# Optimization experiments

Measured on AMD Instinct MI355X. Metric: run time of the kernel, lower is better.

Reference implementation:

```python
import jax, jax.numpy as jnp
import numpy as np

EPS = 1e-9
NEG_BIG = -1e9


def setup_inputs() -> dict:
    key = jax.random.key(0)
    kq, kk, kv, km = jax.random.split(key, 4)
    B, S, D = 2, 2048, 1024
    q = jax.random.normal(kq, (B, S, D), dtype=jnp.float32)
    k = jax.random.normal(kk, (B, S, D), dtype=jnp.float32)
    v = jax.random.normal(kv, (B, S, D), dtype=jnp.float32)
    mask = jax.random.randint(km, (S, S), 0, 2, dtype=jnp.int32)
    return {"q": q, "k": k, "v": v, "mask": mask, "num_heads": 16}


def _split_heads(x, num_heads):
    B, S, D = x.shape
    # [B, S, D] -> [B, H, S, dh]
    return x.reshape(B, S, num_heads, D // num_heads).transpose(0, 2, 1, 3)


def reference(q, k, v, mask, num_heads):
    B, S, D = q.shape
    dh = D // num_heads
    scale = dh ** (-0.5)
    qh = _split_heads(q, num_heads)  # [B,H,S,dh]
    kh = _split_heads(k, num_heads)
    vh = _split_heads(v, num_heads)
    # pairwise euclidean distance (cdist, p=2): sqrt(|q|^2 + |k|^2 - 2 q.k)
    q2 = jnp.sum(qh * qh, axis=-1)  # [B,H,S]
    k2 = jnp.sum(kh * kh, axis=-1)  # [B,H,S]
    qk = jnp.einsum("bhqd,bhkd->bhqk", qh, kh)
    d2 = q2[..., :, None] + k2[..., None, :] - 2.0 * qk
    dist = jnp.sqrt(jnp.maximum(d2, 0.0)) * scale  # [B,H,S,S]
    attn = 1.0 / (dist + EPS)
    attn = attn + mask.astype(jnp.float32)[None, None] * NEG_BIG
    attn = jax.nn.softmax(attn, axis=-1)
    # dropout is identity in eval / p=0.0
    x = jnp.einsum("bhqk,bhkd->bhqd", attn, vh)
    # [B,H,S,dh] -> [B,S,D]
    return x.transpose(0, 2, 1, 3).reshape(B, S, D)
```

## Files before the change

kernel.cpp:

```cpp
#include <hip/hip_runtime.h>
#include <hip/hip_bf16.h>
#include <math.h>

namespace {

constexpr int S  = 2048;
constexpr int D  = 1024;
constexpr int H  = 16;
constexpr int DH = 64;
constexpr int QB = 32;
constexpr int KT = 64;
constexpr float NEG_BIG = -1e9f;

typedef __attribute__((ext_vector_type(8))) short short8;
typedef __attribute__((ext_vector_type(4))) float f32x4;

union Frag {
  unsigned u[4];
  short8 v;
};

constexpr size_t ELEMS   = (size_t)2 * H * S * DH;
constexpr size_t OFF_KHI  = 0;
constexpr size_t OFF_KLO  = ELEMS * 2;
constexpr size_t OFF_VTHI = ELEMS * 4;
constexpr size_t OFF_VTLO = ELEMS * 6;
constexpr size_t OFF_K2   = ELEMS * 8;
constexpr size_t WS_NEED  = ELEMS * 8 + (size_t)2 * H * S * 4;

__device__ __forceinline__ unsigned fbits(float f) { return __float_as_uint(f); }
__device__ __forceinline__ unsigned packhi(unsigned a, unsigned b) {
  return (a >> 16) | (b & 0xFFFF0000u);
}
__device__ __forceinline__ void split2(float e, float o, unsigned& hi, unsigned& lo) {
  const unsigned ue = fbits(e), uo = fbits(o);
  hi = packhi(ue, uo);
  const float he = __uint_as_float(ue & 0xFFFF0000u);
  const float ho = __uint_as_float(uo & 0xFFFF0000u);
  lo = packhi(fbits(e - he), fbits(o - ho));
}

__device__ __forceinline__ unsigned bf16bits(float f) {
  __hip_bfloat16 h = __float2bfloat16(f);
  unsigned short us;
  __builtin_memcpy(&us, &h, 2);
  return (unsigned)us;
}
__device__ __forceinline__ unsigned pk2(float e, float o) {
  return bf16bits(e) | (bf16bits(o) << 16);
}

#define MFMA16 __builtin_amdgcn_mfma_f32_16x16x32_bf16


__global__ __launch_bounds__(256) void prep_k(const float* __restrict__ kin,
                                              short8* __restrict__ khi,
                                              short8* __restrict__ klo,
                                              float* __restrict__ k2) {
  const int t = blockIdx.x * 256 + (int)threadIdx.x;
  const int c = t & 7, h = (t >> 3) & 15, s = (t >> 7) & 2047, b = t >> 18;
  const float* p = kin + ((size_t)(b * S + s)) * D + h * DH + c * 8;
  float f[8];
  *(float4*)f       = *(const float4*)p;
  *(float4*)(f + 4) = *(const float4*)(p + 4);
  Frag hi, lo;
  float ss = 0.f;
#pragma unroll
  for (int w2 = 0; w2 < 4; ++w2) {
    split2(f[2 * w2], f[2 * w2 + 1], hi.u[w2], lo.u[w2]);
    ss += f[2 * w2] * f[2 * w2] + f[2 * w2 + 1] * f[2 * w2 + 1];
  }
  const size_t o8 = ((size_t)((b * 16 + h) * S + s)) * 8 + c;
  khi[o8] = hi.v;
  klo[o8] = lo.v;
  ss += __shfl_xor(ss, 1, 8);
  ss += __shfl_xor(ss, 2, 8);
  ss += __shfl_xor(ss, 4, 8);
  if (c == 0) k2[(b * 16 + h) * S + s] = ss;
}

__global__ __launch_bounds__(256) void prep_vt(const float* __restrict__ vin,
                                               short8* __restrict__ vthi,
                                               short8* __restrict__ vtlo) {
  __shared__ float Vs[64][65];
  const int blk = blockIdx.x;
  const int st = blk & 31, h = (blk >> 5) & 15, b = blk >> 9;
  const int t = (int)threadIdx.x;
  {
    const int r = t >> 2, cq = t & 3;
    const float* p = vin + ((size_t)(b * S + st * 64 + r)) * D + h * DH + cq * 16;
#pragma unroll
    for (int i = 0; i < 4; ++i)
      *(float4*)&Vs[r][cq * 16 + i * 4] = *(const float4*)(p + i * 4);
  }
  __syncthreads();
  const int d = t >> 2, sq = t & 3;
  Frag h0, h1, l0, l1;
#pragma unroll
  for (int j = 0; j < 4; ++j)
    split2(Vs[sq * 16 + 2 * j][d], Vs[sq * 16 + 2 * j + 1][d], h0.u[j], l0.u[j]);
#pragma unroll
  for (int j = 0; j < 4; ++j)
    split2(Vs[sq * 16 + 8 + 2 * j][d], Vs[sq * 16 + 8 + 2 * j + 1][d], h1.u[j], l1.u[j]);
  const size_t o8 = (((size_t)(b * 16 + h) * DH + d) * S + st * 64 + sq * 16) / 8;
  vthi[o8]     = h0.v;
  vthi[o8 + 1] = h1.v;
  vtlo[o8]     = l0.v;
  vtlo[o8 + 1] = l1.v;
}


__global__ __launch_bounds__(256, 2)
void euclid_attn_fast(const float* __restrict__ qg,
                      const int* __restrict__ maskg,
                      const short8* __restrict__ khi,
                      const short8* __restrict__ klo,
                      const short8* __restrict__ vthi,
                      const short8* __restrict__ vtlo,
                      const float* __restrict__ k2g,
                      float* __restrict__ outg) {
  const int bx = blockIdx.x;
  const int bh = blockIdx.y;
  const int b  = bh >> 4;
  const int tid  = (int)threadIdx.x;
  const int w    = tid >> 6;
  const int lane = tid & 63;
  const int x    = lane & 15;
  const int g    = lane >> 4;
  const int q0   = bx * QB;

  const float* Qb = qg + ((size_t)b * S + q0) * D + (bh & 15) * DH;

  const int idxk0 = (20 * g) * 4;
  const int idxe0 = (32 * (g & 1) + x) * 4;

  Frag Qhi[2][2], Qlo[2][2];
  float q2v[2];
#pragma unroll
  for (int nf = 0; nf < 2; ++nf) {
    float ss = 0.f;
#pragma unroll
    for (int s = 0; s < 2; ++s) {
      const float* p = Qb + (16 * nf + x) * D + 32 * s + 8 * g;
      float f[8];
      *(float4*)(f)     = *(const float4*)(p);
      *(float4*)(f + 4) = *(const float4*)(p + 4);
#pragma unroll
      for (int w2 = 0; w2 < 4; ++w2) {
        split2(f[2 * w2], f[2 * w2 + 1], Qhi[nf][s].u[w2], Qlo[nf][s].u[w2]);
        ss += f[2 * w2] * f[2 * w2] + f[2 * w2 + 1] * f[2 * w2 + 1];
      }
    }
    ss += __shfl_xor(ss, 16);
    ss += __shfl_xor(ss, 32);
    q2v[nf] = ss;
  }

  f32x4 acc[2][4] = {};
  float m_[2] = {-1e30f, -1e30f};
  float l_[2] = {0.f, 0.f};

  const int mrow0 = (q0 + x) * S;

  for (int t = 0; t < (S / KT) / 4; ++t) {
    const int k0 = (w + 4 * t) * KT;

    f32x4 dv[4][2];
    float rmax[2] = {-3e38f, -3e38f};

#pragma unroll
    for (int mf = 0; mf < 4; ++mf) {
      float mar[2][4];
#pragma unroll
      for (int nf = 0; nf < 2; ++nf) {
        const int4 mi =
            *(const int4*)(maskg + (size_t)mrow0 + 16 * nf * S + k0 + 16 * mf + 4 * g);
        mar[nf][0] = (float)mi.x; mar[nf][1] = (float)mi.y;
        mar[nf][2] = (float)mi.z; mar[nf][3] = (float)mi.w;
      }

      const size_t kb8 = ((size_t)bh * S + k0 + 16 * mf + x) * 8;
      Frag kh[2], kl[2];
      kh[0].v = khi[kb8 + g];
      kh[1].v = khi[kb8 + 4 + g];
      kl[0].v = klo[kb8 + g];
      kl[1].v = klo[kb8 + 4 + g];

      const float4 k2r = *(const float4*)(k2g + (size_t)bh * S + k0 + 16 * mf + 4 * g);
      const float k2a[4] = {k2r.x, k2r.y, k2r.z, k2r.w};

#pragma unroll
      for (int nf = 0; nf < 2; ++nf) {
        f32x4 d = {0.f, 0.f, 0.f, 0.f};
        d = MFMA16(kl[0].v, Qhi[nf][0].v, d, 0, 0, 0);
        d = MFMA16(kh[0].v, Qlo[nf][0].v, d, 0, 0, 0);
        d = MFMA16(kh[0].v, Qhi[nf][0].v, d, 0, 0, 0);
        d = MFMA16(kl[1].v, Qhi[nf][1].v, d, 0, 0, 0);
        d = MFMA16(kh[1].v, Qlo[nf][1].v, d, 0, 0, 0);
        d = MFMA16(kh[1].v, Qhi[nf][1].v, d, 0, 0, 0);
        dv[mf][nf] = d;
      }

#pragma unroll
      for (int nf = 0; nf < 2; ++nf)
#pragma unroll
        for (int r = 0; r < 4; ++r) {
          float d2 = q2v[nf] + k2a[r] - 2.f * dv[mf][nf][r];
          d2 = fmaxf(d2, 1e-8f);
          float a = 8.f * rsqrtf(d2);
          a = fmaf(mar[nf][r], NEG_BIG, a);
          dv[mf][nf][r] = a;
          rmax[nf] = fmaxf(rmax[nf], a);
        }
    }

    float corr_s[2];
#pragma unroll
    for (int nf = 0; nf < 2; ++nf) {
      float rm = rmax[nf];
      rm = fmaxf(rm, __shfl_xor(rm, 16));
      rm = fmaxf(rm, __shfl_xor(rm, 32));
      float mn   = fmaxf(m_[nf], rm);
      float corr = __expf(m_[nf] - mn);
      m_[nf] = mn;
      float rs = 0.f;
#pragma unroll
      for (int mf = 0; mf < 4; ++mf)
#pragma unroll
        for (int r = 0; r < 4; ++r) {
          float pp = __expf(dv[mf][nf][r] - mn);
          dv[mf][nf][r] = pp;
          rs += pp;
        }
      rs += __shfl_xor(rs, 16);
      rs += __shfl_xor(rs, 32);
      l_[nf] = l_[nf] * corr + rs;
      corr_s[nf] = corr;
    }

#pragma unroll
    for (int mo = 0; mo < 2; ++mo)
#pragma unroll
      for (int r = 0; r < 4; ++r) {
        float cT = __int_as_float(__builtin_amdgcn_ds_bpermute(
            idxk0 + 4 * r, __float_as_int(corr_s[mo])));
#pragma unroll
        for (int nv = 0; nv < 4; ++nv)
          acc[mo][nv][r] *= cT;
      }

    unsigned P2h[2][4][2], P2l[2][4][2];
#pragma unroll
    for (int nf = 0; nf < 2; ++nf)
#pragma unroll
      for (int mf = 0; mf < 4; ++mf)
#pragma unroll
        for (int c = 0; c < 2; ++c)
          split2(dv[mf][nf][2 * c], dv[mf][nf][2 * c + 1],
                 P2h[nf][mf][c], P2l[nf][mf][c]);

    Frag afh[2][2], afl[2][2];
    const bool upper = (g >= 2);
#pragma unroll
    for (int nf = 0; nf < 2; ++nf)
#pragma unroll
      for (int s2 = 0; s2 < 2; ++s2)
#pragma unroll
        for (int w4 = 0; w4 < 4; ++w4) {
          const int c = w4 & 1;
          const int idx = idxe0 + 64 * (w4 >> 1);
          int a0 = __builtin_amdgcn_ds_bpermute(idx, (int)P2h[nf][2 * s2][c]);
          int a1 = __builtin_amdgcn_ds_bpermute(idx, (int)P2h[nf][2 * s2 + 1][c]);
          afh[nf][s2].u[w4] = (unsigned)(upper ? a1 : a0);
          int b0 = __builtin_amdgcn_ds_bpermute(idx, (int)P2l[nf][2 * s2][c]);
          int b1 = __builtin_amdgcn_ds_bpermute(idx, (int)P2l[nf][2 * s2 + 1][c]);
          afl[nf][s2].u[w4] = (unsigned)(upper ? b1 : b0);
        }

#pragma unroll
    for (int nv = 0; nv < 4; ++nv)
#pragma unroll
      for (int s2 = 0; s2 < 2; ++s2) {
        const size_t vt8 =
            (((size_t)bh * DH + 16 * nv + x) * S + k0 + 32 * s2 + 8 * g) / 8;
        Frag vh, vl;
        vh.v = vthi[vt8];
        vl.v = vtlo[vt8];
#pragma unroll
        for (int mo = 0; mo < 2; ++mo) {
          f32x4 a = acc[mo][nv];
          a = MFMA16(afl[mo][s2].v, vh.v, a, 0, 0, 0);
          a = MFMA16(afh[mo][s2].v, vl.v, a, 0, 0, 0);
          a = MFMA16(afh[mo][s2].v, vh.v, a, 0, 0, 0);
          acc[mo][nv] = a;
        }
      }
  }

  __shared__ float accs[4][QB][DH];
  __shared__ float mls[4][2][QB];
#pragma unroll
  for (int mo = 0; mo < 2; ++mo)
#pragma unroll
    for (int nv = 0; nv < 4; ++nv)
#pragma unroll
      for (int r = 0; r < 4; ++r)
        accs[w][16 * mo + 4 * g + r][16 * nv + x] = acc[mo][nv][r];
  if (g == 0) {
#pragma unroll
    for (int nf = 0; nf < 2; ++nf) {
      mls[w][0][16 * nf + x] = m_[nf];
      mls[w][1][16 * nf + x] = l_[nf];
    }
  }
  __syncthreads();

  const int qq  = tid >> 3;
  const int dh0 = (tid & 7) * 8;
  float M = -3e38f;
#pragma unroll
  for (int ww = 0; ww < 4; ++ww) M = fmaxf(M, mls[ww][0][qq]);
  float L = 0.f;
  float sw[4];
#pragma unroll
  for (int ww = 0; ww < 4; ++ww) {
    sw[ww] = __expf(mls[ww][0][qq] - M);
    L += sw[ww] * mls[ww][1][qq];
  }
  const float inv = 1.f / L;
  float o[8] = {};
#pragma unroll
  for (int ww = 0; ww < 4; ++ww)
#pragma unroll
    for (int jj = 0; jj < 8; ++jj)
      o[jj] += sw[ww] * accs[ww][qq][dh0 + jj];
#pragma unroll
  for (int jj = 0; jj < 8; ++jj) o[jj] *= inv;
  float* op = outg + ((size_t)b * S + q0 + qq) * D + (bh & 15) * DH + dh0;
  *(float4*)(op)     = *(float4*)(o);
  *(float4*)(op + 4) = *(float4*)(o + 4);
}


__global__ __launch_bounds__(256, 2)
void euclid_attn_mfma(const float* __restrict__ qg,
                      const float* __restrict__ kg,
                      const float* __restrict__ vg,
                      const int*   __restrict__ maskg,
                      float*       __restrict__ outg) {
  const int bx = blockIdx.x;
  const int bh = blockIdx.y;
  const int b  = bh >> 4, h = bh & 15;
  const int tid  = (int)threadIdx.x;
  const int w    = tid >> 6;
  const int lane = tid & 63;
  const int x    = lane & 15;
  const int g    = lane >> 4;
  const int q0   = bx * QB;

  const float* Qb = qg + ((size_t)b * S + q0) * D + h * DH;
  const float* Kb = kg + (size_t)b * S * D + h * DH;
  const float* Vb = vg + (size_t)b * S * D + h * DH;

  const int idxk0 = (20 * g) * 4;
  const int idxe0 = (32 * (g & 1) + x) * 4;

  Frag Qhi[2][2], Qlo[2][2];
  float q2v[2];
#pragma unroll
  for (int nf = 0; nf < 2; ++nf) {
    float ss = 0.f;
#pragma unroll
    for (int s = 0; s < 2; ++s) {
      const float* p = Qb + (16 * nf + x) * D + 32 * s + 8 * g;
      float f[8];
      *(float4*)(f)     = *(const float4*)(p);
      *(float4*)(f + 4) = *(const float4*)(p + 4);
#pragma unroll
      for (int w2 = 0; w2 < 4; ++w2) {
        float e = f[2*w2], o = f[2*w2+1];
        unsigned hw = pk2(e, o);
        Qhi[nf][s].u[w2] = hw;
        float he = __uint_as_float(hw << 16);
        float ho = __uint_as_float(hw & 0xFFFF0000u);
        Qlo[nf][s].u[w2] = pk2(e - he, o - ho);
        ss += e * e + o * o;
      }
    }
    ss += __shfl_xor(ss, 16);
    ss += __shfl_xor(ss, 32);
    q2v[nf] = ss;
  }

  f32x4 acc[2][4] = {};
  float m_[2] = {-1e30f, -1e30f};
  float l_[2] = {0.f, 0.f};

  const int mrow0 = (q0 + x) * S;

  for (int t = 0; t < (S / KT) / 4; ++t) {
    const int k0 = (w + 4 * t) * KT;

    f32x4 dv[4][2];
    float rmax[2] = {-3e38f, -3e38f};

#pragma unroll
    for (int mf = 0; mf < 4; ++mf) {
      float msk[2][4];
#pragma unroll
      for (int nf = 0; nf < 2; ++nf)
#pragma unroll
        for (int r = 0; r < 4; ++r)
          msk[nf][r] =
              (float)maskg[mrow0 + 16 * nf * S + k0 + 16 * mf + 4 * g + r];

      const float* kp = Kb + (k0 + 16 * mf + x) * D + 8 * g;
      float f[16];
      *(float4*)(f)      = *(const float4*)(kp);
      *(float4*)(f + 4)  = *(const float4*)(kp + 4);
      *(float4*)(f + 8)  = *(const float4*)(kp + 32);
      *(float4*)(f + 12) = *(const float4*)(kp + 36);
      Frag khi[2], klo[2];
      float ss = 0.f;
#pragma unroll
      for (int s = 0; s < 2; ++s)
#pragma unroll
        for (int w2 = 0; w2 < 4; ++w2) {
          float e = f[8*s + 2*w2], o = f[8*s + 2*w2 + 1];
          unsigned hw = pk2(e, o);
          khi[s].u[w2] = hw;
          float he = __uint_as_float(hw << 16);
          float ho = __uint_as_float(hw & 0xFFFF0000u);
          klo[s].u[w2] = pk2(e - he, o - ho);
          ss += e * e + o * o;
        }
      ss += __shfl_xor(ss, 16);
      ss += __shfl_xor(ss, 32);
      float k2r[4];
#pragma unroll
      for (int r = 0; r < 4; ++r)
        k2r[r] = __int_as_float(
            __builtin_amdgcn_ds_bpermute(idxk0 + 4 * r, __float_as_int(ss)));

#pragma unroll
      for (int nf = 0; nf < 2; ++nf) {
        f32x4 d = {0.f, 0.f, 0.f, 0.f};
        d = MFMA16(klo[0].v, Qhi[nf][0].v, d, 0, 0, 0);
        d = MFMA16(khi[0].v, Qlo[nf][0].v, d, 0, 0, 0);
        d = MFMA16(khi[0].v, Qhi[nf][0].v, d, 0, 0, 0);
        d = MFMA16(klo[1].v, Qhi[nf][1].v, d, 0, 0, 0);
        d = MFMA16(khi[1].v, Qlo[nf][1].v, d, 0, 0, 0);
        d = MFMA16(khi[1].v, Qhi[nf][1].v, d, 0, 0, 0);
        dv[mf][nf] = d;
      }

#pragma unroll
      for (int nf = 0; nf < 2; ++nf)
#pragma unroll
        for (int r = 0; r < 4; ++r) {
          float d2 = q2v[nf] + k2r[r] - 2.f * dv[mf][nf][r];
          d2 = fmaxf(d2, 1e-8f);
          float a = 8.f * rsqrtf(d2);
          a = fmaf(msk[nf][r], NEG_BIG, a);
          dv[mf][nf][r] = a;
          rmax[nf] = fmaxf(rmax[nf], a);
        }
    }

    float corr_s[2];
#pragma unroll
    for (int nf = 0; nf < 2; ++nf) {
      float rm = rmax[nf];
      rm = fmaxf(rm, __shfl_xor(rm, 16));
      rm = fmaxf(rm, __shfl_xor(rm, 32));
      float mn   = fmaxf(m_[nf], rm);
      float corr = __expf(m_[nf] - mn);
      m_[nf] = mn;
      float rs = 0.f;
#pragma unroll
      for (int mf = 0; mf < 4; ++mf)
#pragma unroll
        for (int r = 0; r < 4; ++r) {
          float pp = __expf(dv[mf][nf][r] - mn);
          dv[mf][nf][r] = pp;
          rs += pp;
        }
      rs += __shfl_xor(rs, 16);
      rs += __shfl_xor(rs, 32);
      l_[nf] = l_[nf] * corr + rs;
      corr_s[nf] = corr;
    }

#pragma unroll
    for (int mo = 0; mo < 2; ++mo)
#pragma unroll
      for (int r = 0; r < 4; ++r) {
        float cT = __int_as_float(__builtin_amdgcn_ds_bpermute(
            idxk0 + 4 * r, __float_as_int(corr_s[mo])));
#pragma unroll
        for (int nv = 0; nv < 4; ++nv)
          acc[mo][nv][r] *= cT;
      }

    unsigned P2h[2][4][2], P2l[2][4][2];
#pragma unroll
    for (int nf = 0; nf < 2; ++nf)
#pragma unroll
      for (int mf = 0; mf < 4; ++mf)
#pragma unroll
        for (int c = 0; c < 2; ++c) {
          float p0 = dv[mf][nf][2*c], p1 = dv[mf][nf][2*c+1];
          unsigned hw = pk2(p0, p1);
          P2h[nf][mf][c] = hw;
          float he = __uint_as_float(hw << 16);
          float ho = __uint_as_float(hw & 0xFFFF0000u);
          P2l[nf][mf][c] = pk2(p0 - he, p1 - ho);
        }

    Frag afh[2][2], afl[2][2];
    const bool upper = (g >= 2);
#pragma unroll
    for (int nf = 0; nf < 2; ++nf)
#pragma unroll
      for (int s2 = 0; s2 < 2; ++s2)
#pragma unroll
        for (int w4 = 0; w4 < 4; ++w4) {
          const int c = w4 & 1;
          const int idx = idxe0 + 64 * (w4 >> 1);
          int a0 = __builtin_amdgcn_ds_bpermute(idx, (int)P2h[nf][2*s2][c]);
          int a1 = __builtin_amdgcn_ds_bpermute(idx, (int)P2h[nf][2*s2+1][c]);
          afh[nf][s2].u[w4] = (unsigned)(upper ? a1 : a0);
          int b0 = __builtin_amdgcn_ds_bpermute(idx, (int)P2l[nf][2*s2][c]);
          int b1 = __builtin_amdgcn_ds_bpermute(idx, (int)P2l[nf][2*s2+1][c]);
          afl[nf][s2].u[w4] = (unsigned)(upper ? b1 : b0);
        }

#pragma unroll
    for (int nv = 0; nv < 4; ++nv)
#pragma unroll
      for (int s2 = 0; s2 < 2; ++s2) {
        const float* vp = Vb + (k0 + 32 * s2 + 8 * g) * D + 16 * nv + x;
        float f[8];
#pragma unroll
        for (int j = 0; j < 8; ++j) f[j] = vp[j * D];
        Frag vh, vl;
#pragma unroll
        for (int w2 = 0; w2 < 4; ++w2) {
          float e = f[2*w2], o = f[2*w2+1];
          unsigned hw = pk2(e, o);
          vh.u[w2] = hw;
          float he = __uint_as_float(hw << 16);
          float ho = __uint_as_float(hw & 0xFFFF0000u);
          vl.u[w2] = pk2(e - he, o - ho);
        }
#pragma unroll
        for (int mo = 0; mo < 2; ++mo) {
          f32x4 a = acc[mo][nv];
          a = MFMA16(afl[mo][s2].v, vh.v, a, 0, 0, 0);
          a = MFMA16(afh[mo][s2].v, vl.v, a, 0, 0, 0);
          a = MFMA16(afh[mo][s2].v, vh.v, a, 0, 0, 0);
          acc[mo][nv] = a;
        }
      }
  }

  __shared__ float accs[4][QB][DH];
  __shared__ float mls[4][2][QB];
#pragma unroll
  for (int mo = 0; mo < 2; ++mo)
#pragma unroll
    for (int nv = 0; nv < 4; ++nv)
#pragma unroll
      for (int r = 0; r < 4; ++r)
        accs[w][16 * mo + 4 * g + r][16 * nv + x] = acc[mo][nv][r];
  if (g == 0) {
#pragma unroll
    for (int nf = 0; nf < 2; ++nf) {
      mls[w][0][16 * nf + x] = m_[nf];
      mls[w][1][16 * nf + x] = l_[nf];
    }
  }
  __syncthreads();

  const int qq  = tid >> 3;
  const int dh0 = (tid & 7) * 8;
  float M = -3e38f;
#pragma unroll
  for (int ww = 0; ww < 4; ++ww) M = fmaxf(M, mls[ww][0][qq]);
  float L = 0.f;
  float sw[4];
#pragma unroll
  for (int ww = 0; ww < 4; ++ww) {
    sw[ww] = __expf(mls[ww][0][qq] - M);
    L += sw[ww] * mls[ww][1][qq];
  }
  const float inv = 1.f / L;
  float o[8] = {};
#pragma unroll
  for (int ww = 0; ww < 4; ++ww)
#pragma unroll
    for (int jj = 0; jj < 8; ++jj)
      o[jj] += sw[ww] * accs[ww][qq][dh0 + jj];
#pragma unroll
  for (int jj = 0; jj < 8; ++jj) o[jj] *= inv;
  float* op = outg + ((size_t)b * S + q0 + qq) * D + h * DH + dh0;
  *(float4*)(op)     = *(float4*)(o);
  *(float4*)(op + 4) = *(float4*)(o + 4);
}

}

extern "C" void kernel_launch(void* const* d_in, const int* in_sizes, int n_in,
                              void* d_out, int out_size, void* d_ws, size_t ws_size,
                              hipStream_t stream) {
  const float* q    = (const float*)d_in[0];
  const float* k    = (const float*)d_in[1];
  const float* v    = (const float*)d_in[2];
  const int*   mask = (const int*)d_in[3];
  float* out = (float*)d_out;

  const int B = in_sizes[0] / (S * D);
  dim3 grid(S / QB, B * H);
  dim3 block(256);

  if (B == 2 && d_ws != nullptr && ws_size >= WS_NEED) {
    char* ws = (char*)d_ws;
    short8* khi  = (short8*)(ws + OFF_KHI);
    short8* klo  = (short8*)(ws + OFF_KLO);
    short8* vthi = (short8*)(ws + OFF_VTHI);
    short8* vtlo = (short8*)(ws + OFF_VTLO);
    float*  k2   = (float*)(ws + OFF_K2);
    prep_k<<<2048, 256, 0, stream>>>(k, khi, klo, k2);
    prep_vt<<<1024, 256, 0, stream>>>(v, vthi, vtlo);
    euclid_attn_fast<<<grid, block, 0, stream>>>(q, mask, khi, klo, vthi, vtlo,
                                                 k2, out);
  } else {
    euclid_attn_mfma<<<grid, block, 0, stream>>>(q, k, v, mask, out);
  }
}
```

Measured before the change: 413.5 us.

## Use permlane swaps for reductions, lazy softmax rescale, raise occupancy

Replaces shfl_xor reductions and ds_bpermute fragment transposes with permlane32/permlane16 swap builtins when available, so these cross-lane moves avoid LDS-based permutes. Adds a lazy online-softmax rescale that skips updating the running max and rescaling the accumulators unless some row's new max exceeds the old one by more than 8. Raises the launch-bounds occupancy hint from 2 to 4 blocks per SIMD, which limits registers per thread and may cause spills. The lazy threshold keeps the exponent bounded but lets values exceed 1 before normalization.

```diff
diff --git a/kernel.cpp b/kernel.cpp
--- a/kernel.cpp
+++ b/kernel.cpp
@@ -8,7 +8,6 @@
 constexpr int D  = 1024;
 constexpr int H  = 16;
 constexpr int DH = 64;
-constexpr int QB = 32;
 constexpr int KT = 64;
 constexpr float NEG_BIG = -1e9f;
 
@@ -28,6 +27,13 @@
 constexpr size_t OFF_K2   = ELEMS * 8;
 constexpr size_t WS_NEED  = ELEMS * 8 + (size_t)2 * H * S * 4;
 
+#if __has_builtin(__builtin_amdgcn_permlane32_swap) && \
+    __has_builtin(__builtin_amdgcn_permlane16_swap)
+#define HAVE_PLSWAP 1
+#else
+#define HAVE_PLSWAP 0
+#endif
+
 __device__ __forceinline__ unsigned fbits(float f) { return __float_as_uint(f); }
 __device__ __forceinline__ unsigned packhi(unsigned a, unsigned b) {
   return (a >> 16) | (b & 0xFFFF0000u);
@@ -38,6 +44,29 @@
   const float he = __uint_as_float(ue & 0xFFFF0000u);
   const float ho = __uint_as_float(uo & 0xFFFF0000u);
   lo = packhi(fbits(e - he), fbits(o - ho));
+}
+
+__device__ __forceinline__ float red4max(float v) {
+#if HAVE_PLSWAP
+  auto s = __builtin_amdgcn_permlane32_swap(fbits(v), fbits(v), false, false);
+  float a = fmaxf(__uint_as_float(s[0]), __uint_as_float(s[1]));
+  auto t = __builtin_amdgcn_permlane16_swap(fbits(a), fbits(a), false, false);
+  return fmaxf(__uint_as_float(t[0]), __uint_as_float(t[1]));
+#else
+  v = fmaxf(v, __shfl_xor(v, 16));
+  return fmaxf(v, __shfl_xor(v, 32));
+#endif
+}
+__device__ __forceinline__ float red4sum(float v) {
+#if HAVE_PLSWAP
+  auto s = __builtin_amdgcn_permlane32_swap(fbits(v), fbits(v), false, false);
+  float a = __uint_as_float(s[0]) + __uint_as_float(s[1]);
+  auto t = __builtin_amdgcn_permlane16_swap(fbits(a), fbits(a), false, false);
+  return __uint_as_float(t[0]) + __uint_as_float(t[1]);
+#else
+  v += __shfl_xor(v, 16);
+  return v + __shfl_xor(v, 32);
+#endif
 }
 
 __device__ __forceinline__ unsigned bf16bits(float f) {
@@ -110,7 +139,7 @@
 }
 
 
-__global__ __launch_bounds__(256, 2)
+__global__ __launch_bounds__(256, 4)
 void euclid_attn_fast(const float* __restrict__ qg,
                       const int* __restrict__ maskg,
                       const short8* __restrict__ khi,
@@ -127,12 +156,14 @@
   const int lane = tid & 63;
   const int x    = lane & 15;
   const int g    = lane >> 4;
-  const int q0   = bx * QB;
+  const int q0   = bx * 32;
 
   const float* Qb = qg + ((size_t)b * S + q0) * D + (bh & 15) * DH;
 
   const int idxk0 = (20 * g) * 4;
+#if !HAVE_PLSWAP
   const int idxe0 = (32 * (g & 1) + x) * 4;
+#endif
 
   Frag Qhi[2][2], Qlo[2][2];
   float q2v[2];
@@ -151,16 +182,14 @@
         ss += f[2 * w2] * f[2 * w2] + f[2 * w2 + 1] * f[2 * w2 + 1];
       }
     }
-    ss += __shfl_xor(ss, 16);
-    ss += __shfl_xor(ss, 32);
-    q2v[nf] = ss;
+    q2v[nf] = red4sum(ss);
   }
 
   f32x4 acc[2][4] = {};
   float m_[2] = {-1e30f, -1e30f};
   float l_[2] = {0.f, 0.f};
 
-  const int mrow0 = (q0 + x) * S;
+  const size_t mrow0 = (size_t)(q0 + x) * S;
 
   for (int t = 0; t < (S / KT) / 4; ++t) {
     const int k0 = (w + 4 * t) * KT;
@@ -174,7 +203,7 @@
 #pragma unroll
       for (int nf = 0; nf < 2; ++nf) {
         const int4 mi =
-            *(const int4*)(maskg + (size_t)mrow0 + 16 * nf * S + k0 + 16 * mf + 4 * g);
+            *(const int4*)(maskg + mrow0 + 16 * nf * S + k0 + 16 * mf + 4 * g);
         mar[nf][0] = (float)mi.x; mar[nf][1] = (float)mi.y;
         mar[nf][2] = (float)mi.z; mar[nf][3] = (float)mi.w;
       }
@@ -215,39 +244,42 @@
     }
 
     float corr_s[2];
+    bool needr = false;
 #pragma unroll
     for (int nf = 0; nf < 2; ++nf) {
-      float rm = rmax[nf];
-      rm = fmaxf(rm, __shfl_xor(rm, 16));
-      rm = fmaxf(rm, __shfl_xor(rm, 32));
-      float mn   = fmaxf(m_[nf], rm);
-      float corr = __expf(m_[nf] - mn);
-      m_[nf] = mn;
+      const float rm = red4max(rmax[nf]);
+      float corr = 1.f;
+      if (!__all(rm <= m_[nf] + 8.f)) {
+        const float mn = fmaxf(m_[nf], rm);
+        corr = __expf(m_[nf] - mn);
+        m_[nf] = mn;
+        needr = true;
+      }
+      corr_s[nf] = corr;
       float rs = 0.f;
 #pragma unroll
       for (int mf = 0; mf < 4; ++mf)
 #pragma unroll
         for (int r = 0; r < 4; ++r) {
-          float pp = __expf(dv[mf][nf][r] - mn);
+          float pp = __expf(dv[mf][nf][r] - m_[nf]);
           dv[mf][nf][r] = pp;
           rs += pp;
         }
-      rs += __shfl_xor(rs, 16);
-      rs += __shfl_xor(rs, 32);
-      l_[nf] = l_[nf] * corr + rs;
-      corr_s[nf] = corr;
-    }
-
-#pragma unroll
-    for (int mo = 0; mo < 2; ++mo)
-#pragma unroll
-      for (int r = 0; r < 4; ++r) {
-        float cT = __int_as_float(__builtin_amdgcn_ds_bpermute(
-            idxk0 + 4 * r, __float_as_int(corr_s[mo])));
-#pragma unroll
-        for (int nv = 0; nv < 4; ++nv)
-          acc[mo][nv][r] *= cT;
-      }
+      l_[nf] = l_[nf] * corr + red4sum(rs);
+    }
+
+    if (needr) {
+#pragma unroll
+      for (int mo = 0; mo < 2; ++mo)
+#pragma unroll
+        for (int r = 0; r < 4; ++r) {
+          float cT = __int_as_float(__builtin_amdgcn_ds_bpermute(
+              idxk0 + 4 * r, __float_as_int(corr_s[mo])));
+#pragma unroll
+          for (int nv = 0; nv < 4; ++nv)
+            acc[mo][nv][r] *= cT;
+        }
+    }
 
     unsigned P2h[2][4][2], P2l[2][4][2];
 #pragma unroll
@@ -260,6 +292,25 @@
                  P2h[nf][mf][c], P2l[nf][mf][c]);
 
     Frag afh[2][2], afl[2][2];
+#if HAVE_PLSWAP
+#pragma unroll
+    for (int nf = 0; nf < 2; ++nf)
+#pragma unroll
+      for (int s2 = 0; s2 < 2; ++s2)
+#pragma unroll
+        for (int c = 0; c < 2; ++c) {
+          auto sh = __builtin_amdgcn_permlane32_swap(
+              P2h[nf][2 * s2][c], P2h[nf][2 * s2 + 1][c], false, false);
+          auto th = __builtin_amdgcn_permlane16_swap(sh[0], sh[1], false, false);
+          afh[nf][s2].u[c]     = th[0];
+          afh[nf][s2].u[c + 2] = th[1];
+          auto sl = __builtin_amdgcn_permlane32_swap(
+              P2l[nf][2 * s2][c], P2l[nf][2 * s2 + 1][c], false, false);
+          auto tl = __builtin_amdgcn_permlane16_swap(sl[0], sl[1], false, false);
+          afl[nf][s2].u[c]     = tl[0];
+          afl[nf][s2].u[c + 2] = tl[1];
+        }
+#else
     const bool upper = (g >= 2);
 #pragma unroll
     for (int nf = 0; nf < 2; ++nf)
@@ -269,13 +320,14 @@
         for (int w4 = 0; w4 < 4; ++w4) {
           const int c = w4 & 1;
           const int idx = idxe0 + 64 * (w4 >> 1);
-          int a0 = __builtin_amdgcn_ds_bpermute(idx, (int)P2h[nf][2 * s2][c]);
-          int a1 = __builtin_amdgcn_ds_bpermute(idx, (int)P2h[nf][2 * s2 + 1][c]);
+          int a0 = __builtin_amdgcn_ds_bpermute(idx, (int)P2h[nf][2*s2][c]);
+          int a1 = __builtin_amdgcn_ds_bpermute(idx, (int)P2h[nf][2*s2+1][c]);
           afh[nf][s2].u[w4] = (unsigned)(upper ? a1 : a0);
-          int b0 = __builtin_amdgcn_ds_bpermute(idx, (int)P2l[nf][2 * s2][c]);
-          int b1 = __builtin_amdgcn_ds_bpermute(idx, (int)P2l[nf][2 * s2 + 1][c]);
+          int b0 = __builtin_amdgcn_ds_bpermute(idx, (int)P2l[nf][2*s2][c]);
+          int b1 = __builtin_amdgcn_ds_bpermute(idx, (int)P2l[nf][2*s2+1][c]);
           afl[nf][s2].u[w4] = (unsigned)(upper ? b1 : b0);
         }
+#endif
 
 #pragma unroll
     for (int nv = 0; nv < 4; ++nv)
@@ -297,8 +349,8 @@
       }
   }
 
-  __shared__ float accs[4][QB][DH];
-  __shared__ float mls[4][2][QB];
+  __shared__ float accs[4][32][DH];
+  __shared__ float mls[4][2][32];
 #pragma unroll
   for (int mo = 0; mo < 2; ++mo)
 #pragma unroll
@@ -356,7 +408,7 @@
   const int lane = tid & 63;
   const int x    = lane & 15;
   const int g    = lane >> 4;
-  const int q0   = bx * QB;
+  const int q0   = bx * 32;
 
   const float* Qb = qg + ((size_t)b * S + q0) * D + h * DH;
   const float* Kb = kg + (size_t)b * S * D + h * DH;
@@ -564,8 +616,8 @@
       }
   }
 
-  __shared__ float accs[4][QB][DH];
-  __shared__ float mls[4][2][QB];
+  __shared__ float accs[4][32][DH];
+  __shared__ float mls[4][2][32];
 #pragma unroll
   for (int mo = 0; mo < 2; ++mo)
 #pragma unroll
@@ -620,7 +672,7 @@
   float* out = (float*)d_out;
 
   const int B = in_sizes[0] / (S * D);
-  dim3 grid(S / QB, B * H);
+  dim3 grid(S / 32, B * H);
   dim3 block(256);
 
   if (B == 2 && d_ws != nullptr && ws_size >= WS_NEED) {
```

Measured after the change: 535.3 us. 1.29x slower.
